# Kernel optimization log

Measured on AMD Instinct MI355X. Metric: run time of the kernel, lower is better.

Reference implementation:

```python
import jax, jax.numpy as jnp
import numpy as np

NUM_EXPERT = 16
IN_FEAT = 1024
OUT_FEAT = 1024
BATCH = 8192


def setup_inputs() -> dict:
    key = jax.random.key(0)
    k_inp, k_gate, k_w = jax.random.split(key, 3)
    inp = jax.random.normal(k_inp, (BATCH, IN_FEAT), dtype=jnp.float32)
    gate = jax.random.randint(k_gate, (BATCH,), 0, NUM_EXPERT, dtype=jnp.int32)
    # nn.Linear default init: uniform(-1/sqrt(in_feat), 1/sqrt(in_feat))
    bound = 1.0 / np.sqrt(IN_FEAT)
    weight = jax.random.uniform(
        k_w, (NUM_EXPERT, OUT_FEAT, IN_FEAT), dtype=jnp.float32,
        minval=-bound, maxval=bound)
    return {"inp": inp, "gate": gate, "weight": weight}


def reference(inp, gate, weight):
    # o[t] = weight[gate[t]] @ inp[t]
    # Loop over the (small, fixed) expert axis via lax.scan; each step does a
    # dense [B, in] @ [in, out] GEMM and keeps rows routed to that expert.
    num_expert, out_feat, _ = weight.shape
    batch = inp.shape[0]

    def body(o, xs):
        i, w = xs  # w: [out_feat, in_feat]
        y = inp @ w.T  # [batch, out_feat]
        sel = (gate == i)[:, None]
        return jnp.where(sel, y, o), None

    o0 = jnp.zeros((batch, out_feat), dtype=inp.dtype)
    o, _ = jax.lax.scan(body, o0, (jnp.arange(num_expert), weight))
    return o
```

## Files before the change

kernel.cpp:

```cpp
#include <hip/hip_runtime.h>
#include <hip/hip_bf16.h>

#define NE    16
#define KDIM  1024
#define NDIM  1024
#define BATCH 8192
#define TM    128
#define TN    128
#define MAXT  96

typedef __attribute__((ext_vector_type(8))) short short8;
typedef __attribute__((ext_vector_type(4))) float floatx4;
typedef unsigned short ushort_t;

#define O_CNT  0
#define O_OFF  64
#define O_TG0  256
#define O_TE   1024
#define O_TEND 2048
#define O_POS  4096
#define O_TOK  36864
#define O_PA   73728
#define O_W    17113088
#define WS_REQ 50667520

#define GLOAD_LDS(gp, lp) __builtin_amdgcn_global_load_lds( \
    (const __attribute__((address_space(1))) unsigned int*)(gp), \
    (__attribute__((address_space(3))) unsigned int*)(lp), 16, 0, 0)

__device__ __forceinline__ unsigned int pk2bf(float x, float y) {
    __hip_bfloat162 h = __float22bfloat162_rn(make_float2(x, y));
    unsigned int u;
    __builtin_memcpy(&u, &h, 4);
    return u;
}


__global__ void zero_k(int* cnt) {
    if (threadIdx.x < NE) cnt[threadIdx.x] = 0;
}

__global__ void hist_k(const int* __restrict__ gate, int* cnt, int* pos) {
    int t = blockIdx.x * blockDim.x + threadIdx.x;
    if (t < BATCH) pos[t] = atomicAdd(&cnt[gate[t]], 1);
}

__global__ void scan_k(const int* __restrict__ cnt, int* off,
                       int* tg0, int* te, int* tend) {
    if (threadIdx.x == 0) {
        int o = 0, nt = 0;
        off[0] = 0;
        for (int e = 0; e < NE; ++e) {
            int c = cnt[e];
            for (int r = 0; r < c; r += TM) {
                int r0 = (r + TM <= c) ? r : (c > TM ? c - TM : 0);
                tg0[nt] = o + r0; te[nt] = e; tend[nt] = o + c; ++nt;
            }
            o += c; off[e + 1] = o;
        }
        for (; nt < MAXT; ++nt) { tg0[nt] = 0; te[nt] = 0; tend[nt] = 0; }
    }
}

__global__ __launch_bounds__(256) void prep_k(
        const float* __restrict__ inp, const float* __restrict__ wgt,
        const int* __restrict__ gate, const int* __restrict__ pos,
        const int* __restrict__ off, ushort_t* __restrict__ pA,
        ushort_t* __restrict__ pW, int* __restrict__ tok) {
    int b = blockIdx.x, tid = threadIdx.x;
    if (b < BATCH) {
        int t = b;
        int g = off[gate[t]] + pos[t];
        float4 v = *(const float4*)&inp[(size_t)t * KDIM + tid * 4];
        uint2 u = make_uint2(pk2bf(v.x, v.y), pk2bf(v.z, v.w));
        *(uint2*)&pA[(size_t)g * KDIM + tid * 4] = u;
        if (tid == 0) tok[g] = t;
    } else {
        size_t i = (size_t)(b - BATCH) * 1024 + tid * 4;
        float4 v = *(const float4*)&wgt[i];
        uint2 u = make_uint2(pk2bf(v.x, v.y), pk2bf(v.z, v.w));
        *(uint2*)&pW[i] = u;
    }
}

__global__ __launch_bounds__(256) void moe_gemm2_k(
        const ushort_t* __restrict__ pA, const ushort_t* __restrict__ pW,
        const int* __restrict__ tg0, const int* __restrict__ teArr,
        const int* __restrict__ tend, const int* __restrict__ tok,
        float* __restrict__ out) {
    const int y   = blockIdx.y;
    const int g0  = tg0[y];
    const int end = tend[y];
    if (g0 >= end) return;
    const int e    = teArr[y];
    const int out0 = blockIdx.x * TN;

    __shared__ ushort_t As[2][TM][32];
    __shared__ ushort_t Bs[2][TN][32];
    __shared__ int tok_s[TM];

    const int tid = threadIdx.x;
    if (tid < TM) tok_s[tid] = tok[g0 + tid];

    const int wave = tid >> 6, lane = tid & 63;
    const int wm = (wave >> 1) * 64, wn = (wave & 1) * 64;
    const int quad = lane >> 4, l16 = lane & 15;

    const ushort_t* Ab = pA + (size_t)g0 * KDIM;
    const ushort_t* Bb = pW + (size_t)e * (KDIM * NDIM) + (size_t)out0 * KDIM;

    floatx4 acc[4][4] = {};
    const int c0 = wave * 64 + lane;

    for (int k0 = 0; k0 < KDIM; k0 += 64) {
        __syncthreads();
        #pragma unroll
        for (int i = 0; i < 4; ++i) {
            int c = c0 + i * 256;
            int half = c >> 9, row = (c >> 2) & 127, kc = c & 3;
            int goff = row * KDIM + k0 + half * 32 + kc * 8;
            int cb = (i * 4 + wave) * 64;
            GLOAD_LDS(Ab + goff, (ushort_t*)As + (size_t)cb * 8);
        }
        #pragma unroll
        for (int i = 0; i < 4; ++i) {
            int c = c0 + i * 256;
            int half = c >> 9, row = (c >> 2) & 127, kc = c & 3;
            int goff = row * KDIM + k0 + half * 32 + kc * 8;
            int cb = (i * 4 + wave) * 64;
            GLOAD_LDS(Bb + goff, (ushort_t*)Bs + (size_t)cb * 8);
        }
        __syncthreads();

        #pragma unroll
        for (int s = 0; s < 2; ++s) {
            short8 a[4], b[4];
            #pragma unroll
            for (int i = 0; i < 4; ++i)
                a[i] = *(const short8*)&As[s][wm + i * 16 + l16][quad * 8];
            #pragma unroll
            for (int i = 0; i < 4; ++i)
                b[i] = *(const short8*)&Bs[s][wn + i * 16 + l16][quad * 8];
            #pragma unroll
            for (int mi = 0; mi < 4; ++mi)
                #pragma unroll
                for (int ni = 0; ni < 4; ++ni)
                    acc[mi][ni] = __builtin_amdgcn_mfma_f32_16x16x32_bf16(
                        a[mi], b[ni], acc[mi][ni], 0, 0, 0);
        }
    }

    #pragma unroll
    for (int mi = 0; mi < 4; ++mi) {
        #pragma unroll
        for (int r = 0; r < 4; ++r) {
            int lrow = wm + mi * 16 + quad * 4 + r;
            if (g0 + lrow < end) {
                int t = tok_s[lrow];
                float* orow = out + (size_t)t * NDIM + out0 + wn + l16;
                #pragma unroll
                for (int ni = 0; ni < 4; ++ni)
                    orow[ni * 16] = acc[mi][ni][r];
            }
        }
    }
}

#define LDW 20
__global__ void bin_tokens_k(const int* __restrict__ gate, int* cnt, int* idx) {
    int t = blockIdx.x * blockDim.x + threadIdx.x;
    if (t < BATCH) {
        int e = gate[t];
        int p = atomicAdd(&cnt[e], 1);
        idx[e * BATCH + p] = t;
    }
}

__global__ __launch_bounds__(256) void moe_gemm_k(
        const float* __restrict__ inp, const float* __restrict__ wgt,
        const int* __restrict__ cnt, const int* __restrict__ idx,
        float* __restrict__ out) {
    const int e = blockIdx.z;
    const int n_e = cnt[e];
    const int row0 = blockIdx.y * TM;
    if (row0 >= n_e) return;
    const int out0 = blockIdx.x * TN;
    __shared__ unsigned int As[TM * LDW];
    __shared__ unsigned int Bs[TN * LDW];
    __shared__ int tok_s[TM];
    const int tid = threadIdx.x;
    if (tid < TM) {
        int g = row0 + tid;
        tok_s[tid] = (g < n_e) ? idx[e * BATCH + g] : -1;
    }
    const int wave = tid >> 6, lane = tid & 63;
    const int wm = (wave >> 1) * 64, wn = (wave & 1) * 64;
    const int quad = lane >> 4, l16 = lane & 15;
    floatx4 acc[4][4] = {};
    const int cg = (tid & 7) * 4;
    const int rbase = tid >> 3;
    const float* wbase = wgt + (size_t)e * KDIM * NDIM;
    for (int k0 = 0; k0 < KDIM; k0 += 32) {
        __syncthreads();
        #pragma unroll
        for (int p = 0; p < 4; ++p) {
            int row = p * 32 + rbase;
            int t = tok_s[row];
            float4 va = make_float4(0.f, 0.f, 0.f, 0.f);
            if (t >= 0) va = *(const float4*)&inp[(size_t)t * KDIM + k0 + cg];
            As[row * LDW + (cg >> 1)]     = pk2bf(va.x, va.y);
            As[row * LDW + (cg >> 1) + 1] = pk2bf(va.z, va.w);
            float4 vb = *(const float4*)&wbase[(size_t)(out0 + row) * KDIM + k0 + cg];
            Bs[row * LDW + (cg >> 1)]     = pk2bf(vb.x, vb.y);
            Bs[row * LDW + (cg >> 1) + 1] = pk2bf(vb.z, vb.w);
        }
        __syncthreads();
        short8 a[4], b[4];
        #pragma unroll
        for (int i = 0; i < 4; ++i)
            a[i] = *(const short8*)&As[(wm + i * 16 + l16) * LDW + quad * 4];
        #pragma unroll
        for (int i = 0; i < 4; ++i)
            b[i] = *(const short8*)&Bs[(wn + i * 16 + l16) * LDW + quad * 4];
        #pragma unroll
        for (int mi = 0; mi < 4; ++mi)
            #pragma unroll
            for (int ni = 0; ni < 4; ++ni)
                acc[mi][ni] = __builtin_amdgcn_mfma_f32_16x16x32_bf16(
                    a[mi], b[ni], acc[mi][ni], 0, 0, 0);
    }
    #pragma unroll
    for (int mi = 0; mi < 4; ++mi) {
        #pragma unroll
        for (int r = 0; r < 4; ++r) {
            int lrow = wm + mi * 16 + quad * 4 + r;
            int t = tok_s[lrow];
            if (t >= 0) {
                float* orow = out + (size_t)t * NDIM + out0 + wn + l16;
                #pragma unroll
                for (int ni = 0; ni < 4; ++ni)
                    orow[ni * 16] = acc[mi][ni][r];
            }
        }
    }
}

extern "C" void kernel_launch(void* const* d_in, const int* in_sizes, int n_in,
                              void* d_out, int out_size, void* d_ws, size_t ws_size,
                              hipStream_t stream) {
    const float* inp  = (const float*)d_in[0];
    const int*   gate = (const int*)d_in[1];
    const float* wgt  = (const float*)d_in[2];
    float*       out  = (float*)d_out;
    char* w = (char*)d_ws;

    if (ws_size >= WS_REQ) {
        int* cnt  = (int*)(w + O_CNT);
        int* off  = (int*)(w + O_OFF);
        int* tg0  = (int*)(w + O_TG0);
        int* te   = (int*)(w + O_TE);
        int* tend = (int*)(w + O_TEND);
        int* pos  = (int*)(w + O_POS);
        int* tok  = (int*)(w + O_TOK);
        ushort_t* pA = (ushort_t*)(w + O_PA);
        ushort_t* pW = (ushort_t*)(w + O_W);

        zero_k<<<1, 64, 0, stream>>>(cnt);
        hist_k<<<BATCH / 256, 256, 0, stream>>>(gate, cnt, pos);
        scan_k<<<1, 64, 0, stream>>>(cnt, off, tg0, te, tend);
        prep_k<<<BATCH + NE * 1024, 256, 0, stream>>>(inp, wgt, gate, pos, off,
                                                      pA, pW, tok);
        dim3 grid(NDIM / TN, MAXT, 1);
        moe_gemm2_k<<<grid, 256, 0, stream>>>(pA, pW, tg0, te, tend, tok, out);
    } else {
        int* cnt = (int*)d_ws;
        int* idx = cnt + NE;
        zero_k<<<1, 64, 0, stream>>>(cnt);
        bin_tokens_k<<<BATCH / 256, 256, 0, stream>>>(gate, cnt, idx);
        dim3 grid(NDIM / TN, BATCH / TM, NE);
        moe_gemm_k<<<grid, 256, 0, stream>>>(inp, wgt, cnt, idx, out);
    }
}
```

Before: 198.8 us.

## Double-buffer grouped MoE GEMM with async LDS prefetch and narrower N tile

Replaces the GEMM's load-then-compute loop with a double-buffered pipeline. The next 32-wide K slice is fetched into the alternate LDS buffer with global_load_lds while MFMAs run on the current one, which also cuts one barrier per step. The N tile drops from 128 to 64 and launch bounds ask for 4 blocks per CU, doubling grid size for better occupancy at the cost of less B reuse per block. The tile-building scan kernel now runs one thread per expert instead of a single serial thread.

```diff
diff --git a/kernel.cpp b/kernel.cpp
--- a/kernel.cpp
+++ b/kernel.cpp
@@ -6,7 +6,7 @@
 #define NDIM  1024
 #define BATCH 8192
 #define TM    128
-#define TN    128
+#define TN    64
 #define MAXT  96
 
 typedef __attribute__((ext_vector_type(8))) short short8;
@@ -47,18 +47,26 @@
 
 __global__ void scan_k(const int* __restrict__ cnt, int* off,
                        int* tg0, int* te, int* tend) {
-    if (threadIdx.x == 0) {
-        int o = 0, nt = 0;
-        off[0] = 0;
-        for (int e = 0; e < NE; ++e) {
-            int c = cnt[e];
-            for (int r = 0; r < c; r += TM) {
-                int r0 = (r + TM <= c) ? r : (c > TM ? c - TM : 0);
-                tg0[nt] = o + r0; te[nt] = e; tend[nt] = o + c; ++nt;
-            }
-            o += c; off[e + 1] = o;
-        }
-        for (; nt < MAXT; ++nt) { tg0[nt] = 0; te[nt] = 0; tend[nt] = 0; }
+    __shared__ int ntot;
+    int t = threadIdx.x;
+    if (t < NE) {
+        int o = 0, ts = 0;
+        for (int j = 0; j < NE; ++j) {
+            int c = cnt[j];
+            if (j < t) { o += c; ts += (c + TM - 1) / TM; }
+        }
+        int c = cnt[t];
+        off[t] = o;
+        if (t == NE - 1) { off[NE] = o + c; ntot = ts + (c + TM - 1) / TM; }
+        int nt = ts;
+        for (int r = 0; r < c; r += TM) {
+            int r0 = (r + TM <= c) ? r : (c > TM ? c - TM : 0);
+            tg0[nt] = o + r0; te[nt] = t; tend[nt] = o + c; ++nt;
+        }
+    }
+    __syncthreads();
+    for (int i = ntot + t; i < MAXT; i += 64) {
+        tg0[i] = 0; te[i] = 0; tend[i] = 0;
     }
 }
 
@@ -83,7 +91,7 @@
     }
 }
 
-__global__ __launch_bounds__(256) void moe_gemm2_k(
+__global__ __launch_bounds__(256, 4) void moe_gemm3_k(
         const ushort_t* __restrict__ pA, const ushort_t* __restrict__ pW,
         const int* __restrict__ tg0, const int* __restrict__ teArr,
         const int* __restrict__ tend, const int* __restrict__ tok,
@@ -103,51 +111,56 @@
     if (tid < TM) tok_s[tid] = tok[g0 + tid];
 
     const int wave = tid >> 6, lane = tid & 63;
-    const int wm = (wave >> 1) * 64, wn = (wave & 1) * 64;
+    const int wm = (wave >> 1) * 64;
+    const int wn = (wave & 1) * 32;
     const int quad = lane >> 4, l16 = lane & 15;
 
     const ushort_t* Ab = pA + (size_t)g0 * KDIM;
     const ushort_t* Bb = pW + (size_t)e * (KDIM * NDIM) + (size_t)out0 * KDIM;
 
-    floatx4 acc[4][4] = {};
-    const int c0 = wave * 64 + lane;
-
-    for (int k0 = 0; k0 < KDIM; k0 += 64) {
+    floatx4 acc[4][2] = {};
+
+    const int cA0 = wave * 64 + lane;
+    const int cB  = wave * 64 + lane;
+
+    {
+        #pragma unroll
+        for (int i = 0; i < 2; ++i) {
+            int c = cA0 + i * 256;
+            GLOAD_LDS(Ab + (c >> 2) * KDIM + (c & 3) * 8,
+                      (ushort_t*)As[0] + (size_t)(i * 256 + wave * 64) * 8);
+        }
+        GLOAD_LDS(Bb + (cB >> 2) * KDIM + (cB & 3) * 8,
+                  (ushort_t*)Bs[0] + (size_t)(wave * 64) * 8);
+    }
+
+    int buf = 0;
+    for (int k0 = 0; k0 < KDIM; k0 += 32, buf ^= 1) {
         __syncthreads();
-        #pragma unroll
-        for (int i = 0; i < 4; ++i) {
-            int c = c0 + i * 256;
-            int half = c >> 9, row = (c >> 2) & 127, kc = c & 3;
-            int goff = row * KDIM + k0 + half * 32 + kc * 8;
-            int cb = (i * 4 + wave) * 64;
-            GLOAD_LDS(Ab + goff, (ushort_t*)As + (size_t)cb * 8);
-        }
-        #pragma unroll
-        for (int i = 0; i < 4; ++i) {
-            int c = c0 + i * 256;
-            int half = c >> 9, row = (c >> 2) & 127, kc = c & 3;
-            int goff = row * KDIM + k0 + half * 32 + kc * 8;
-            int cb = (i * 4 + wave) * 64;
-            GLOAD_LDS(Bb + goff, (ushort_t*)Bs + (size_t)cb * 8);
-        }
-        __syncthreads();
-
-        #pragma unroll
-        for (int s = 0; s < 2; ++s) {
-            short8 a[4], b[4];
+        if (k0 + 32 < KDIM) {
+            int kn = k0 + 32;
             #pragma unroll
-            for (int i = 0; i < 4; ++i)
-                a[i] = *(const short8*)&As[s][wm + i * 16 + l16][quad * 8];
+            for (int i = 0; i < 2; ++i) {
+                int c = cA0 + i * 256;
+                GLOAD_LDS(Ab + (c >> 2) * KDIM + kn + (c & 3) * 8,
+                          (ushort_t*)As[buf ^ 1] + (size_t)(i * 256 + wave * 64) * 8);
+            }
+            GLOAD_LDS(Bb + (cB >> 2) * KDIM + kn + (cB & 3) * 8,
+                      (ushort_t*)Bs[buf ^ 1] + (size_t)(wave * 64) * 8);
+        }
+        short8 a[4], b[2];
+        #pragma unroll
+        for (int i = 0; i < 4; ++i)
+            a[i] = *(const short8*)&As[buf][wm + i * 16 + l16][quad * 8];
+        #pragma unroll
+        for (int i = 0; i < 2; ++i)
+            b[i] = *(const short8*)&Bs[buf][wn + i * 16 + l16][quad * 8];
+        #pragma unroll
+        for (int mi = 0; mi < 4; ++mi)
             #pragma unroll
-            for (int i = 0; i < 4; ++i)
-                b[i] = *(const short8*)&Bs[s][wn + i * 16 + l16][quad * 8];
-            #pragma unroll
-            for (int mi = 0; mi < 4; ++mi)
-                #pragma unroll
-                for (int ni = 0; ni < 4; ++ni)
-                    acc[mi][ni] = __builtin_amdgcn_mfma_f32_16x16x32_bf16(
-                        a[mi], b[ni], acc[mi][ni], 0, 0, 0);
-        }
+            for (int ni = 0; ni < 2; ++ni)
+                acc[mi][ni] = __builtin_amdgcn_mfma_f32_16x16x32_bf16(
+                    a[mi], b[ni], acc[mi][ni], 0, 0, 0);
     }
 
     #pragma unroll
@@ -159,7 +172,7 @@
                 int t = tok_s[lrow];
                 float* orow = out + (size_t)t * NDIM + out0 + wn + l16;
                 #pragma unroll
-                for (int ni = 0; ni < 4; ++ni)
+                for (int ni = 0; ni < 2; ++ni)
                     orow[ni * 16] = acc[mi][ni][r];
             }
         }
@@ -184,9 +197,9 @@
     const int n_e = cnt[e];
     const int row0 = blockIdx.y * TM;
     if (row0 >= n_e) return;
-    const int out0 = blockIdx.x * TN;
+    const int out0 = blockIdx.x * 128;
     __shared__ unsigned int As[TM * LDW];
-    __shared__ unsigned int Bs[TN * LDW];
+    __shared__ unsigned int Bs[TM * LDW];
     __shared__ int tok_s[TM];
     const int tid = threadIdx.x;
     if (tid < TM) {
@@ -271,13 +284,13 @@
         prep_k<<<BATCH + NE * 1024, 256, 0, stream>>>(inp, wgt, gate, pos, off,
                                                       pA, pW, tok);
         dim3 grid(NDIM / TN, MAXT, 1);
-        moe_gemm2_k<<<grid, 256, 0, stream>>>(pA, pW, tg0, te, tend, tok, out);
+        moe_gemm3_k<<<grid, 256, 0, stream>>>(pA, pW, tg0, te, tend, tok, out);
     } else {
         int* cnt = (int*)d_ws;
         int* idx = cnt + NE;
         zero_k<<<1, 64, 0, stream>>>(cnt);
         bin_tokens_k<<<BATCH / 256, 256, 0, stream>>>(gate, cnt, idx);
-        dim3 grid(NDIM / TN, BATCH / TM, NE);
+        dim3 grid(NDIM / 128, BATCH / TM, NE);
         moe_gemm_k<<<grid, 256, 0, stream>>>(inp, wgt, cnt, idx, out);
     }
 }
```

Result: no change. 199.8 us (+0.5%).
